# Kernel optimization log

Hardware: AMD Instinct MI355X
Metric: run time of the kernel (lower is better)

## Reference

```python
import jax, jax.numpy as jnp
import numpy as np

B, C, H, W = 8, 64, 56, 56
PLANES = 64
EPS = 1e-5


def conv2d(x, w, b, stride=1, pad=1):
    out = jax.lax.conv_general_dilated(
        x, w, window_strides=(stride, stride), padding=[(pad, pad), (pad, pad)],
        dimension_numbers=('NCHW', 'OIHW', 'NCHW'))
    return out + b[None, :, None, None]


def _bilinear_gather(img, py, px):
    # img: [C,H,W]; py/px: [K2,Ho,Wo] float sample coords; zero outside bounds
    Ci, Hi, Wi = img.shape
    y0 = jnp.floor(py); x0 = jnp.floor(px)
    wy1 = py - y0; wx1 = px - x0
    wy0 = 1.0 - wy1; wx0 = 1.0 - wx1

    def g(yc, xc):
        valid = ((yc >= 0) & (yc < Hi) & (xc >= 0) & (xc < Wi)).astype(img.dtype)
        yi = jnp.clip(yc, 0, Hi - 1).astype(jnp.int32)
        xi = jnp.clip(xc, 0, Wi - 1).astype(jnp.int32)
        return img[:, yi, xi] * valid[None]  # [C,K2,Ho,Wo]

    return (g(y0, x0) * (wy0 * wx0)[None] + g(y0, x0 + 1) * (wy0 * wx1)[None]
            + g(y0 + 1, x0) * (wy1 * wx0)[None] + g(y0 + 1, x0 + 1) * (wy1 * wx1)[None])


def deform_conv2d(x, offset, weight, stride, pad, dil):
    # torchvision DeformConv2d semantics (no mask). offset: [B, 2*K2, Ho, Wo]
    Bx, Cx, Hx, Wx = x.shape
    O, _, kh, kw = weight.shape
    K2 = kh * kw
    Ho, Wo = offset.shape[2], offset.shape[3]
    off = offset.reshape(Bx, K2, 2, Ho, Wo)
    dy, dx = off[:, :, 0], off[:, :, 1]
    ki, kj = jnp.meshgrid(jnp.arange(kh), jnp.arange(kw), indexing='ij')
    base_y = (ki.reshape(-1) * dil - pad).astype(x.dtype)  # [K2]
    base_x = (kj.reshape(-1) * dil - pad).astype(x.dtype)
    hg = (jnp.arange(Ho) * stride).astype(x.dtype)
    wg = (jnp.arange(Wo) * stride).astype(x.dtype)
    py = dy + base_y[None, :, None, None] + hg[None, None, :, None]
    px = dx + base_x[None, :, None, None] + wg[None, None, None, :]
    cols = jax.vmap(_bilinear_gather)(x, py, px)  # [B,C,K2,Ho,Wo]
    return jnp.einsum('bckhw,ock->bohw', cols, weight.reshape(O, Cx, K2))


def bn(x, gamma, beta, mean, var):
    inv = gamma / jnp.sqrt(var + EPS)
    return x * inv[None, :, None, None] + (beta - mean * inv)[None, :, None, None]


def setup_inputs() -> dict:
    key = jax.random.key(0)
    ks = jax.random.split(key, 12)
    s = 0.05
    d = {
        'x':   jax.random.normal(ks[0], (B, C, H, W), jnp.float32),
        'ow1': jax.random.normal(ks[1], (2 * 9, C, 3, 3), jnp.float32) * s,
        'ob1': jnp.zeros((2 * 9,), jnp.float32),
        'ow3': jax.random.normal(ks[2], (2 * 25, C, 3, 3), jnp.float32) * s,
        'ob3': jnp.zeros((2 * 25,), jnp.float32),
        'ow2': jax.random.normal(ks[3], (2 * 9, PLANES, 3, 3), jnp.float32) * s,
        'ob2': jnp.zeros((2 * 9,), jnp.float32),
        'w1':  jax.random.normal(ks[4], (PLANES, C, 3, 3), jnp.float32) * s,
        'w3':  jax.random.normal(ks[5], (PLANES, C, 5, 5), jnp.float32) * s,
        'w2':  jax.random.normal(ks[6], (PLANES, PLANES, 3, 3), jnp.float32) * s,
    }
    for i, tag in zip((7, 8, 9), ('1', '3', '2')):
        d['g' + tag] = jnp.ones((PLANES,), jnp.float32)
        d['b' + tag] = jnp.zeros((PLANES,), jnp.float32)
        d['m' + tag] = jax.random.normal(ks[i], (PLANES,), jnp.float32) * 0.1
        d['v' + tag] = jnp.ones((PLANES,), jnp.float32)
    return d


def reference(x, ow1, ob1, ow3, ob3, ow2, ob2, w1, w3, w2,
              g1, b1, m1, v1, g3, b3, m3, v3, g2, b2, m2, v2):
    offset1 = conv2d(x, ow1, ob1, stride=1, pad=1)
    out = jax.nn.relu(bn(deform_conv2d(x, offset1, w1, 1, 2, 2), g1, b1, m1, v1))
    offset3 = conv2d(x, ow3, ob3, stride=1, pad=1)
    out_1 = jax.nn.relu(bn(deform_conv2d(x, offset3, w3, 1, 4, 2), g3, b3, m3, v3))
    out = out + out_1
    offset2 = conv2d(out, ow2, ob2, stride=1, pad=1)
    out = bn(deform_conv2d(out, offset2, w2, 1, 2, 2), g2, b2, m2, v2)
    out = out + x  # identity shortcut (stride=1, in_planes==planes)
    return jax.nn.relu(out)
```

## Files before the change

### kernel.cpp

```cpp
#include <hip/hip_runtime.h>
#include <math.h>

#define HD 56
#define WD 56
#define CD 64
#define PLANE 3136

typedef _Float16 f16x8 __attribute__((ext_vector_type(8)));
typedef _Float16 f16x4 __attribute__((ext_vector_type(4)));
typedef _Float16 f16x2 __attribute__((ext_vector_type(2)));
typedef float    f32x4 __attribute__((ext_vector_type(4)));

__global__ __launch_bounds__(256) void wtrans_k(
    const float* __restrict__ w1, const float* __restrict__ w3, const float* __restrict__ w2,
    const float* __restrict__ ow1, const float* __restrict__ ow3, const float* __restrict__ ow2,
    _Float16* __restrict__ t1, _Float16* __restrict__ t3, _Float16* __restrict__ t2,
    _Float16* __restrict__ owF, _Float16* __restrict__ owT2)
{
    int y = blockIdx.y;
    if (y == 0 || y == 1 || y == 2) {
        const float* src = (y == 0) ? w1 : (y == 1) ? w3 : w2;
        _Float16* dst    = (y == 0) ? t1 : (y == 1) ? t3 : t2;
        int K2 = (y == 1) ? 25 : 9;
        int total = 64 * 64 * K2;
        for (int idx = blockIdx.x * 256 + threadIdx.x; idx < total; idx += gridDim.x * 256) {
            int k = idx >> 12;
            int o = (idx >> 6) & 63;
            int c = idx & 63;
            dst[idx] = (_Float16)src[(o * 64 + c) * K2 + k];
        }
    } else if (y == 3) {
        int total = 9 * 32 * 64;
        for (int idx = blockIdx.x * 256 + threadIdx.x; idx < total; idx += gridDim.x * 256) {
            int k = idx >> 11;
            int o = (idx >> 6) & 31;
            int c = idx & 63;
            owF[k * 6144 + o * 64 + c] = (o < 18) ? (_Float16)ow1[(o * 64 + c) * 9 + k] : (_Float16)0.f;
        }
    } else if (y == 4) {
        int total = 9 * 64 * 64;
        for (int idx = blockIdx.x * 256 + threadIdx.x; idx < total; idx += gridDim.x * 256) {
            int k = idx >> 12;
            int o = (idx >> 6) & 63;
            int c = idx & 63;
            owF[k * 6144 + (32 + o) * 64 + c] = (o < 50) ? (_Float16)ow3[(o * 64 + c) * 9 + k] : (_Float16)0.f;
        }
    } else {
        int total = 9 * 32 * 64;
        for (int idx = blockIdx.x * 256 + threadIdx.x; idx < total; idx += gridDim.x * 256) {
            int k = idx >> 11;
            int o = (idx >> 6) & 31;
            int c = idx & 63;
            owT2[k * 2048 + o * 64 + c] = (o < 18) ? (_Float16)ow2[(o * 64 + c) * 9 + k] : (_Float16)0.f;
        }
    }
}

__global__ __launch_bounds__(256) void xt_k(const float* __restrict__ src, _Float16* __restrict__ dst)
{
    int b  = blockIdx.y;
    int px = blockIdx.x * 64 + (threadIdx.x & 63);
    int cg = threadIdx.x >> 6;
    const float* s = src + (size_t)b * CD * PLANE + px;
    f16x8 lo, hi;
#pragma unroll
    for (int i = 0; i < 8; ++i) lo[i] = (_Float16)s[(cg * 16 + i) * PLANE];
#pragma unroll
    for (int i = 0; i < 8; ++i) hi[i] = (_Float16)s[(cg * 16 + 8 + i) * PLANE];
    _Float16* d = dst + ((size_t)b * PLANE + px) * 64 + cg * 16;
    *(f16x8*)d = lo;
    *(f16x8*)(d + 8) = hi;
}

template<int NTILES, int OP>
__device__ inline void af_load(const _Float16* __restrict__ ow, int k, int off, f16x8* s) {
    const _Float16* wk = ow + k * (OP * 64);
#pragma unroll
    for (int t = 0; t < NTILES; ++t) s[t] = *(const f16x8*)(wk + (t * 16) * 64 + off);
}

template<int FUSED>
__global__ __launch_bounds__(256) void offc_k(
    const _Float16* __restrict__ src,
    const _Float16* __restrict__ ow,
    const float* __restrict__ biasA, const float* __restrict__ biasB,
    uint4* __restrict__ tbl)
{
    constexpr int NTILES = FUSED ? 6 : 2;
    constexpr int OP     = FUSED ? 96 : 32;
    constexpr int NTT    = FUSED ? 34 : 9;
    __shared__ float red[4][NTILES * 4 * 64];

    int tid = threadIdx.x;
    int bid = blockIdx.x;
    int b    = bid & 7;
    int tile = bid >> 3;
    int l = tid & 63;
    int n = l & 15;
    int g = l >> 4;
    int w = tid >> 6;
    int tg = w >> 1;
    int pix = tile * 16 + n;
    int ho = pix / WD, wo = pix - ho * WD;
    int ckoff = (w & 1) * 32 + g * 8;
    int afo = n * 64 + ckoff;
    const _Float16* sp = src + ((size_t)b * PLANE + pix) * 64 + ckoff;

    f32x4 acc[NTILES];
#pragma unroll
    for (int t = 0; t < NTILES; ++t) acc[t] = (f32x4){0.f, 0.f, 0.f, 0.f};

#define NB(K, D) { int ky_=(K)/3-1, kx_=(K)%3-1; int yn_=ho+ky_, xn_=wo+kx_;       \
    f16x8 z_ = {(_Float16)0,(_Float16)0,(_Float16)0,(_Float16)0,                   \
                (_Float16)0,(_Float16)0,(_Float16)0,(_Float16)0};                  \
    D = z_;                                                                        \
    if ((unsigned)yn_ < (unsigned)HD && (unsigned)xn_ < (unsigned)WD)              \
        D = *(const f16x8*)(sp + (ky_ * WD + kx_) * 64); }

#define MFMAS(S, NBV) { _Pragma("unroll")                                          \
    for (int t = 0; t < NTILES; ++t)                                               \
        acc[t] = __builtin_amdgcn_mfma_f32_16x16x32_f16((S)[t], NBV, acc[t], 0, 0, 0); }

    f16x8 sA[NTILES], sB[NTILES];
    if (tg == 0) {
        f16x8 nb0, nb1, nb2, nb3, nb4;
        NB(0, nb0) NB(1, nb1) NB(2, nb2) NB(3, nb3) NB(4, nb4)
        af_load<NTILES, OP>(ow, 0, afo, sA);
        af_load<NTILES, OP>(ow, 1, afo, sB); MFMAS(sA, nb0)
        af_load<NTILES, OP>(ow, 2, afo, sA); MFMAS(sB, nb1)
        af_load<NTILES, OP>(ow, 3, afo, sB); MFMAS(sA, nb2)
        af_load<NTILES, OP>(ow, 4, afo, sA); MFMAS(sB, nb3)
        MFMAS(sA, nb4)
    } else {
        f16x8 nb0, nb1, nb2, nb3;
        NB(5, nb0) NB(6, nb1) NB(7, nb2) NB(8, nb3)
        af_load<NTILES, OP>(ow, 5, afo, sA);
        af_load<NTILES, OP>(ow, 6, afo, sB); MFMAS(sA, nb0)
        af_load<NTILES, OP>(ow, 7, afo, sA); MFMAS(sB, nb1)
        af_load<NTILES, OP>(ow, 8, afo, sB); MFMAS(sA, nb2)
        MFMAS(sB, nb3)
    }
#undef NB
#undef MFMAS

#pragma unroll
    for (int t = 0; t < NTILES; ++t)
#pragma unroll
        for (int rr = 0; rr < 4; ++rr)
            red[w][(t * 4 + rr) * 64 + l] = acc[t][rr];
    __syncthreads();

#pragma unroll
    for (int tt = 0; tt < (NTILES + 3) / 4; ++tt) {
        int t = w + tt * 4;
        if (t < NTILES) {
            float v[4];
#pragma unroll
            for (int rr = 0; rr < 4; ++rr) {
                int ia = (t * 4 + rr) * 64 + l;
                v[rr] = red[0][ia] + red[1][ia] + red[2][ia] + red[3][ia];
            }
            int obase = t * 16 + g * 4;
            bool isB = FUSED && (t >= 2);
            int oc0 = isB ? (obase - 32) : obase;
            const float* bp = isB ? biasB : biasA;
#pragma unroll
            for (int pp = 0; pp < 2; ++pp) {
                int oce = oc0 + pp * 2;
                int kl  = oce >> 1;
                int kmax = isB ? 25 : 9;
                if (kl < kmax) {
                    float dy = v[pp * 2]     + bp[oce];
                    float dx = v[pp * 2 + 1] + bp[oce + 1];
                    int by, bx;
                    if (isB) { int q = kl / 5; by = q * 2 - 4; bx = (kl - q * 5) * 2 - 4; }
                    else     { int q = kl / 3; by = q * 2 - 2; bx = (kl - q * 3) * 2 - 2; }
                    float py = dy + (float)(by + ho);
                    float px = dx + (float)(bx + wo);
                    float fy = floorf(py), fx = floorf(px);
                    float wy1 = py - fy, wx1 = px - fx;
                    float wy0 = 1.f - wy1, wx0 = 1.f - wx1;
                    int y0 = (int)fy, x0 = (int)fx;
                    int y1 = y0 + 1, x1 = x0 + 1;
                    float vy0 = (y0 >= 0 && y0 < HD) ? 1.f : 0.f;
                    float vy1 = (y1 >= 0 && y1 < HD) ? 1.f : 0.f;
                    float vx0 = (x0 >= 0 && x0 < WD) ? 1.f : 0.f;
                    float vx1 = (x1 >= 0 && x1 < WD) ? 1.f : 0.f;
                    int cy0 = min(max(y0, 0), HD - 1), cy1 = min(max(y1, 0), HD - 1);
                    int cx0 = min(max(x0, 0), WD - 1), cx1 = min(max(x1, 0), WD - 1);
                    unsigned i00 = (unsigned)(cy0 * WD + cx0), i01 = (unsigned)(cy0 * WD + cx1);
                    unsigned i10 = (unsigned)(cy1 * WD + cx0), i11 = (unsigned)(cy1 * WD + cx1);
                    f16x2 wl = {(_Float16)(wy0 * wx0 * vy0 * vx0), (_Float16)(wy0 * wx1 * vy0 * vx1)};
                    f16x2 wh = {(_Float16)(wy1 * wx0 * vy1 * vx0), (_Float16)(wy1 * wx1 * vy1 * vx1)};
                    uint4 e;
                    e.x = i00 | (i01 << 16);
                    e.y = i10 | (i11 << 16);
                    e.z = __builtin_bit_cast(unsigned int, wl);
                    e.w = __builtin_bit_cast(unsigned int, wh);
                    int gtap = isB ? (9 + kl) : kl;
                    tbl[((size_t)(b * NTT + gtap)) * PLANE + pix] = e;
                }
            }
        }
    }
}

template<int MERGED>
__global__ __launch_bounds__(512) void dconv_k(
    const _Float16* __restrict__ xt,
    const uint4* __restrict__ tbl,
    const _Float16* __restrict__ wTA, const _Float16* __restrict__ wTB,
    const float* __restrict__ gA, const float* __restrict__ bA,
    const float* __restrict__ mA, const float* __restrict__ vA,
    const float* __restrict__ gB, const float* __restrict__ bB,
    const float* __restrict__ mB, const float* __restrict__ vB,
    const float* __restrict__ addsrc, float* __restrict__ out,
    _Float16* __restrict__ outh)
{
    constexpr int NT = MERGED ? 34 : 9;
    constexpr int RS = MERGED ? 32 : 16;
    __shared__ float red[2][3][RS * 64];

    int tid = threadIdx.x;
    int bid = blockIdx.x;
    int b    = bid & 7;
    int tp2  = bid >> 3;
    int l   = tid & 63;
    int n   = l & 15;
    int g   = l >> 4;
    int w   = tid >> 6;
    int pr  = w & 1;
    int kh  = (w >> 1) & 1;
    int tg  = w >> 2;
    int tile = tp2 * 2 + pr;
    int pix = tile * 16 + n;
    int ckoff = kh * 32 + g * 8;

    int base, cnt;
    if (MERGED) { base = tg * 17; cnt = 17; }
    else        { base = tg ? 5 : 0; cnt = tg ? 4 : 5; }

    const _Float16* xp = xt + (size_t)b * PLANE * 64 + ckoff;
    const uint4*    tp = tbl + (size_t)b * NT * PLANE + pix;
    int afoff = n * 64 + ckoff;

    f32x4 accA[4], accB[4];
#pragma unroll
    for (int ot = 0; ot < 4; ++ot) {
        accA[ot] = (f32x4){0.f, 0.f, 0.f, 0.f};
        accB[ot] = (f32x4){0.f, 0.f, 0.f, 0.f};
    }

    f16x8 v00, v01, v10, v11, af0, af1, af2, af3;
    _Float16 w0, w1, w2, w3;
    uint4 e_cur;

    {
        uint4 e0 = tp[base * PLANE];
        int t1 = (cnt > 1) ? base + 1 : base;
        e_cur = tp[t1 * PLANE];
        unsigned i00 = e0.x & 0xffffu, i01 = e0.x >> 16;
        unsigned i10 = e0.y & 0xffffu, i11 = e0.y >> 16;
        v00 = *(const f16x8*)(xp + i00 * 64);
        v01 = *(const f16x8*)(xp + i01 * 64);
        v10 = *(const f16x8*)(xp + i10 * 64);
        v11 = *(const f16x8*)(xp + i11 * 64);
        const _Float16* wk = (!MERGED || base < 9) ? (wTA + base * 4096) : (wTB + (base - 9) * 4096);
        af0 = *(const f16x8*)(wk + afoff);
        af1 = *(const f16x8*)(wk + afoff + 1024);
        af2 = *(const f16x8*)(wk + afoff + 2048);
        af3 = *(const f16x8*)(wk + afoff + 3072);
        f16x2 wl = __builtin_bit_cast(f16x2, e0.z);
        f16x2 wh = __builtin_bit_cast(f16x2, e0.w);
        w0 = wl.x; w1 = wl.y; w2 = wh.x; w3 = wh.y;
    }

#pragma unroll 2
    for (int j = 0; j < cnt; ++j) {
        int tap = base + j;
        bool hn = (j + 1 < cnt);
        f16x8 nv00, nv01, nv10, nv11, naf0, naf1, naf2, naf3;
        uint4 e_nxt;
        if (hn) {
            int t2 = (j + 2 < cnt) ? (tap + 2) : (base + cnt - 1);
            e_nxt = tp[t2 * PLANE];
            unsigned i00 = e_cur.x & 0xffffu, i01 = e_cur.x >> 16;
            unsigned i10 = e_cur.y & 0xffffu, i11 = e_cur.y >> 16;
            nv00 = *(const f16x8*)(xp + i00 * 64);
            nv01 = *(const f16x8*)(xp + i01 * 64);
            nv10 = *(const f16x8*)(xp + i10 * 64);
            nv11 = *(const f16x8*)(xp + i11 * 64);
            const _Float16* wk = (!MERGED || tap + 1 < 9) ? (wTA + (tap + 1) * 4096)
                                                          : (wTB + (tap - 8) * 4096);
            naf0 = *(const f16x8*)(wk + afoff);
            naf1 = *(const f16x8*)(wk + afoff + 1024);
            naf2 = *(const f16x8*)(wk + afoff + 2048);
            naf3 = *(const f16x8*)(wk + afoff + 3072);
        }
        f16x8 bf = v00 * w0 + v01 * w1 + v10 * w2 + v11 * w3;
        if (!MERGED || tap < 9) {
            accA[0] = __builtin_amdgcn_mfma_f32_16x16x32_f16(af0, bf, accA[0], 0, 0, 0);
            accA[1] = __builtin_amdgcn_mfma_f32_16x16x32_f16(af1, bf, accA[1], 0, 0, 0);
            accA[2] = __builtin_amdgcn_mfma_f32_16x16x32_f16(af2, bf, accA[2], 0, 0, 0);
            accA[3] = __builtin_amdgcn_mfma_f32_16x16x32_f16(af3, bf, accA[3], 0, 0, 0);
        } else {
            accB[0] = __builtin_amdgcn_mfma_f32_16x16x32_f16(af0, bf, accB[0], 0, 0, 0);
            accB[1] = __builtin_amdgcn_mfma_f32_16x16x32_f16(af1, bf, accB[1], 0, 0, 0);
            accB[2] = __builtin_amdgcn_mfma_f32_16x16x32_f16(af2, bf, accB[2], 0, 0, 0);
            accB[3] = __builtin_amdgcn_mfma_f32_16x16x32_f16(af3, bf, accB[3], 0, 0, 0);
        }
        if (hn) {
            v00 = nv00; v01 = nv01; v10 = nv10; v11 = nv11;
            af0 = naf0; af1 = naf1; af2 = naf2; af3 = naf3;
            f16x2 wl = __builtin_bit_cast(f16x2, e_cur.z);
            f16x2 wh = __builtin_bit_cast(f16x2, e_cur.w);
            w0 = wl.x; w1 = wl.y; w2 = wh.x; w3 = wh.y;
            e_cur = e_nxt;
        }
    }

    int pidx = (tg << 1) | kh;
    if (pidx > 0) {
#pragma unroll
        for (int ot = 0; ot < 4; ++ot)
#pragma unroll
            for (int rr = 0; rr < 4; ++rr) {
                red[pr][pidx - 1][(ot * 4 + rr) * 64 + l] = accA[ot][rr];
                if (MERGED) red[pr][pidx - 1][(16 + ot * 4 + rr) * 64 + l] = accB[ot][rr];
            }
    }
    __syncthreads();
    if (pidx == 0) {
#pragma unroll
        for (int ot = 0; ot < 4; ++ot) {
            float r[4];
#pragma unroll
            for (int rr = 0; rr < 4; ++rr) {
                int ia = (ot * 4 + rr) * 64 + l;
                int o = ot * 16 + g * 4 + rr;
                if (MERGED) {
                    int ib = (16 + ot * 4 + rr) * 64 + l;
                    float sumA = accA[ot][rr] + red[pr][0][ia] + red[pr][1][ia] + red[pr][2][ia];
                    float sumB = accB[ot][rr] + red[pr][0][ib] + red[pr][1][ib] + red[pr][2][ib];
                    float ivA = gA[o] * (1.f / sqrtf(vA[o] + 1e-5f));
                    float shA = bA[o] - mA[o] * ivA;
                    float ivB = gB[o] * (1.f / sqrtf(vB[o] + 1e-5f));
                    float shB = bB[o] - mB[o] * ivB;
                    r[rr] = fmaxf(sumA * ivA + shA, 0.f) + fmaxf(sumB * ivB + shB, 0.f);
                } else {
                    float s = accA[ot][rr] + red[pr][0][ia] + red[pr][1][ia] + red[pr][2][ia];
                    float iv = gA[o] * (1.f / sqrtf(vA[o] + 1e-5f));
                    float sh = bA[o] - mA[o] * iv;
                    size_t oidx = (size_t)(b * 64 + o) * PLANE + pix;
                    out[oidx] = fmaxf(s * iv + sh + addsrc[oidx], 0.f);
                }
            }
            if (MERGED) {
                f16x4 hv = {(_Float16)r[0], (_Float16)r[1], (_Float16)r[2], (_Float16)r[3]};
                *(f16x4*)(outh + ((size_t)b * PLANE + pix) * 64 + ot * 16 + g * 4) = hv;
            }
        }
    }
}

extern "C" void kernel_launch(void* const* d_in, const int* in_sizes, int n_in,
                              void* d_out, int out_size, void* d_ws, size_t ws_size,
                              hipStream_t stream) {
    const float* x   = (const float*)d_in[0];
    const float* ow1 = (const float*)d_in[1];
    const float* ob1 = (const float*)d_in[2];
    const float* ow3 = (const float*)d_in[3];
    const float* ob3 = (const float*)d_in[4];
    const float* ow2 = (const float*)d_in[5];
    const float* ob2 = (const float*)d_in[6];
    const float* w1  = (const float*)d_in[7];
    const float* w3  = (const float*)d_in[8];
    const float* w2  = (const float*)d_in[9];
    const float* g1  = (const float*)d_in[10];
    const float* b1  = (const float*)d_in[11];
    const float* m1  = (const float*)d_in[12];
    const float* v1  = (const float*)d_in[13];
    const float* g3  = (const float*)d_in[14];
    const float* b3  = (const float*)d_in[15];
    const float* m3  = (const float*)d_in[16];
    const float* v3  = (const float*)d_in[17];
    const float* g2  = (const float*)d_in[18];
    const float* b2  = (const float*)d_in[19];
    const float* m2  = (const float*)d_in[20];
    const float* v2  = (const float*)d_in[21];

    float* out = (float*)d_out;
    float* ws  = (float*)d_ws;

    _Float16* xth  = (_Float16*)ws;
    _Float16* mth  = (_Float16*)(ws + 802816);
    uint4*    tbl  = (uint4*)(ws + 1605632);
    _Float16* wT1h = (_Float16*)(ws + 5017600);
    _Float16* wT3h = wT1h + 36864;
    _Float16* wT2h = wT3h + 102400;
    _Float16* owFh = wT2h + 36864;
    _Float16* owT2h= owFh + 55296;

    wtrans_k<<<dim3(16, 6), dim3(256), 0, stream>>>(
        w1, w3, w2, ow1, ow3, ow2, wT1h, wT3h, wT2h, owFh, owT2h);
    xt_k<<<dim3(49, 8), dim3(256), 0, stream>>>(x, xth);

    offc_k<1><<<dim3(1568), dim3(256), 0, stream>>>(xth, owFh, ob1, ob3, tbl);

    dconv_k<1><<<dim3(784), dim3(512), 0, stream>>>(
        xth, tbl, wT1h, wT3h, g1, b1, m1, v1, g3, b3, m3, v3, nullptr, nullptr, mth);

    offc_k<0><<<dim3(1568), dim3(256), 0, stream>>>(mth, owT2h, ob2, ob2, tbl);

    dconv_k<0><<<dim3(784), dim3(512), 0, stream>>>(
        mth, tbl, wT2h, wT2h, g2, b2, m2, v2, g2, b2, m2, v2, x, out, nullptr);
}
```

Baseline: 219.3 us.

## Process two pixel tiles per wave to reuse weight fragments across MFMAs

Each wave in the deformable conv kernel now handles two 16-pixel tiles and shares one set of loaded weight A-fragments between them, halving weight loads per MFMA. Block sizes drop to 384 and 256 threads. The merged kernel splits taps unevenly (9, 12 and 13) so that each wave group accumulates only branch A or only branch B, which removes the dual accumulator set. This costs more registers per thread for the doubled gathered values and accumulators, and there are fewer waves per block to hide gather latency.

```diff
diff --git a/kernel.cpp b/kernel.cpp
--- a/kernel.cpp
+++ b/kernel.cpp
@@ -206,7 +206,7 @@
 }
 
 template<int MERGED>
-__global__ __launch_bounds__(512) void dconv_k(
+__global__ __launch_bounds__(MERGED ? 384 : 256) void dconv_k(
     const _Float16* __restrict__ xt,
     const uint4* __restrict__ tbl,
     const _Float16* __restrict__ wTA, const _Float16* __restrict__ wTB,
@@ -218,146 +218,154 @@
     _Float16* __restrict__ outh)
 {
     constexpr int NT = MERGED ? 34 : 9;
-    constexpr int RS = MERGED ? 32 : 16;
-    __shared__ float red[2][3][RS * 64];
+    constexpr int NP = MERGED ? 5 : 3;
+    __shared__ float red[NP][2][16 * 64];
 
     int tid = threadIdx.x;
     int bid = blockIdx.x;
     int b    = bid & 7;
     int tp2  = bid >> 3;
-    int l   = tid & 63;
-    int n   = l & 15;
-    int g   = l >> 4;
-    int w   = tid >> 6;
-    int pr  = w & 1;
-    int kh  = (w >> 1) & 1;
-    int tg  = w >> 2;
-    int tile = tp2 * 2 + pr;
-    int pix = tile * 16 + n;
+    int l = tid & 63, n = l & 15, g = l >> 4;
+    int w = tid >> 6;
+    int kh = w & 1;
+    int tg = w >> 1;
+    int pix0 = tp2 * 32 + n;
     int ckoff = kh * 32 + g * 8;
 
     int base, cnt;
-    if (MERGED) { base = tg * 17; cnt = 17; }
-    else        { base = tg ? 5 : 0; cnt = tg ? 4 : 5; }
+    bool isA;
+    if (MERGED) {
+        base = (tg == 0) ? 0 : (tg == 1) ? 9 : 21;
+        cnt  = (tg == 0) ? 9 : (tg == 1) ? 12 : 13;
+        isA  = (tg == 0);
+    } else {
+        base = tg ? 5 : 0; cnt = tg ? 4 : 5; isA = true;
+    }
+    const _Float16* wTb = isA ? wTA : wTB;
+    int kofs = isA ? 0 : 9;
 
     const _Float16* xp = xt + (size_t)b * PLANE * 64 + ckoff;
-    const uint4*    tp = tbl + (size_t)b * NT * PLANE + pix;
+    const uint4* tpp = tbl + (size_t)b * NT * PLANE + pix0;
     int afoff = n * 64 + ckoff;
 
-    f32x4 accA[4], accB[4];
-#pragma unroll
-    for (int ot = 0; ot < 4; ++ot) {
-        accA[ot] = (f32x4){0.f, 0.f, 0.f, 0.f};
-        accB[ot] = (f32x4){0.f, 0.f, 0.f, 0.f};
-    }
-
-    f16x8 v00, v01, v10, v11, af0, af1, af2, af3;
-    _Float16 w0, w1, w2, w3;
-    uint4 e_cur;
+    f32x4 acc[2][4];
+#pragma unroll
+    for (int t = 0; t < 2; ++t)
+#pragma unroll
+        for (int q = 0; q < 4; ++q) acc[t][q] = (f32x4){0.f, 0.f, 0.f, 0.f};
+
+    f16x8 v[2][4], af4[4];
+    uint4 ecur[2];
+    unsigned wz[2], ww[2];
 
     {
-        uint4 e0 = tp[base * PLANE];
+        uint4 e00 = tpp[base * PLANE];
+        uint4 e01 = tpp[base * PLANE + 16];
         int t1 = (cnt > 1) ? base + 1 : base;
-        e_cur = tp[t1 * PLANE];
-        unsigned i00 = e0.x & 0xffffu, i01 = e0.x >> 16;
-        unsigned i10 = e0.y & 0xffffu, i11 = e0.y >> 16;
-        v00 = *(const f16x8*)(xp + i00 * 64);
-        v01 = *(const f16x8*)(xp + i01 * 64);
-        v10 = *(const f16x8*)(xp + i10 * 64);
-        v11 = *(const f16x8*)(xp + i11 * 64);
-        const _Float16* wk = (!MERGED || base < 9) ? (wTA + base * 4096) : (wTB + (base - 9) * 4096);
-        af0 = *(const f16x8*)(wk + afoff);
-        af1 = *(const f16x8*)(wk + afoff + 1024);
-        af2 = *(const f16x8*)(wk + afoff + 2048);
-        af3 = *(const f16x8*)(wk + afoff + 3072);
-        f16x2 wl = __builtin_bit_cast(f16x2, e0.z);
-        f16x2 wh = __builtin_bit_cast(f16x2, e0.w);
-        w0 = wl.x; w1 = wl.y; w2 = wh.x; w3 = wh.y;
+        ecur[0] = tpp[t1 * PLANE];
+        ecur[1] = tpp[t1 * PLANE + 16];
+        uint4 ee[2] = {e00, e01};
+#pragma unroll
+        for (int t = 0; t < 2; ++t) {
+            unsigned i00 = ee[t].x & 0xffffu, i01 = ee[t].x >> 16;
+            unsigned i10 = ee[t].y & 0xffffu, i11 = ee[t].y >> 16;
+            v[t][0] = *(const f16x8*)(xp + i00 * 64);
+            v[t][1] = *(const f16x8*)(xp + i01 * 64);
+            v[t][2] = *(const f16x8*)(xp + i10 * 64);
+            v[t][3] = *(const f16x8*)(xp + i11 * 64);
+            wz[t] = ee[t].z; ww[t] = ee[t].w;
+        }
+        const _Float16* wk = wTb + (base - kofs) * 4096;
+#pragma unroll
+        for (int q = 0; q < 4; ++q) af4[q] = *(const f16x8*)(wk + afoff + q * 1024);
     }
 
 #pragma unroll 2
     for (int j = 0; j < cnt; ++j) {
         int tap = base + j;
         bool hn = (j + 1 < cnt);
-        f16x8 nv00, nv01, nv10, nv11, naf0, naf1, naf2, naf3;
-        uint4 e_nxt;
+        f16x8 nv[2][4], naf[4];
+        uint4 enxt[2];
         if (hn) {
             int t2 = (j + 2 < cnt) ? (tap + 2) : (base + cnt - 1);
-            e_nxt = tp[t2 * PLANE];
-            unsigned i00 = e_cur.x & 0xffffu, i01 = e_cur.x >> 16;
-            unsigned i10 = e_cur.y & 0xffffu, i11 = e_cur.y >> 16;
-            nv00 = *(const f16x8*)(xp + i00 * 64);
-            nv01 = *(const f16x8*)(xp + i01 * 64);
-            nv10 = *(const f16x8*)(xp + i10 * 64);
-            nv11 = *(const f16x8*)(xp + i11 * 64);
-            const _Float16* wk = (!MERGED || tap + 1 < 9) ? (wTA + (tap + 1) * 4096)
-                                                          : (wTB + (tap - 8) * 4096);
-            naf0 = *(const f16x8*)(wk + afoff);
-            naf1 = *(const f16x8*)(wk + afoff + 1024);
-            naf2 = *(const f16x8*)(wk + afoff + 2048);
-            naf3 = *(const f16x8*)(wk + afoff + 3072);
-        }
-        f16x8 bf = v00 * w0 + v01 * w1 + v10 * w2 + v11 * w3;
-        if (!MERGED || tap < 9) {
-            accA[0] = __builtin_amdgcn_mfma_f32_16x16x32_f16(af0, bf, accA[0], 0, 0, 0);
-            accA[1] = __builtin_amdgcn_mfma_f32_16x16x32_f16(af1, bf, accA[1], 0, 0, 0);
-            accA[2] = __builtin_amdgcn_mfma_f32_16x16x32_f16(af2, bf, accA[2], 0, 0, 0);
-            accA[3] = __builtin_amdgcn_mfma_f32_16x16x32_f16(af3, bf, accA[3], 0, 0, 0);
-        } else {
-            accB[0] = __builtin_amdgcn_mfma_f32_16x16x32_f16(af0, bf, accB[0], 0, 0, 0);
-            accB[1] = __builtin_amdgcn_mfma_f32_16x16x32_f16(af1, bf, accB[1], 0, 0, 0);
-            accB[2] = __builtin_amdgcn_mfma_f32_16x16x32_f16(af2, bf, accB[2], 0, 0, 0);
-            accB[3] = __builtin_amdgcn_mfma_f32_16x16x32_f16(af3, bf, accB[3], 0, 0, 0);
+            enxt[0] = tpp[t2 * PLANE];
+            enxt[1] = tpp[t2 * PLANE + 16];
+#pragma unroll
+            for (int t = 0; t < 2; ++t) {
+                unsigned i00 = ecur[t].x & 0xffffu, i01 = ecur[t].x >> 16;
+                unsigned i10 = ecur[t].y & 0xffffu, i11 = ecur[t].y >> 16;
+                nv[t][0] = *(const f16x8*)(xp + i00 * 64);
+                nv[t][1] = *(const f16x8*)(xp + i01 * 64);
+                nv[t][2] = *(const f16x8*)(xp + i10 * 64);
+                nv[t][3] = *(const f16x8*)(xp + i11 * 64);
+            }
+            const _Float16* wk = wTb + (tap + 1 - kofs) * 4096;
+#pragma unroll
+            for (int q = 0; q < 4; ++q) naf[q] = *(const f16x8*)(wk + afoff + q * 1024);
+        }
+#pragma unroll
+        for (int t = 0; t < 2; ++t) {
+            f16x2 wl = __builtin_bit_cast(f16x2, wz[t]);
+            f16x2 wh = __builtin_bit_cast(f16x2, ww[t]);
+            f16x8 bf = v[t][0] * wl.x + v[t][1] * wl.y + v[t][2] * wh.x + v[t][3] * wh.y;
+#pragma unroll
+            for (int q = 0; q < 4; ++q)
+                acc[t][q] = __builtin_amdgcn_mfma_f32_16x16x32_f16(af4[q], bf, acc[t][q], 0, 0, 0);
         }
         if (hn) {
-            v00 = nv00; v01 = nv01; v10 = nv10; v11 = nv11;
-            af0 = naf0; af1 = naf1; af2 = naf2; af3 = naf3;
-            f16x2 wl = __builtin_bit_cast(f16x2, e_cur.z);
-            f16x2 wh = __builtin_bit_cast(f16x2, e_cur.w);
-            w0 = wl.x; w1 = wl.y; w2 = wh.x; w3 = wh.y;
-            e_cur = e_nxt;
-        }
-    }
-
-    int pidx = (tg << 1) | kh;
-    if (pidx > 0) {
-#pragma unroll
-        for (int ot = 0; ot < 4; ++ot)
-#pragma unroll
-            for (int rr = 0; rr < 4; ++rr) {
-                red[pr][pidx - 1][(ot * 4 + rr) * 64 + l] = accA[ot][rr];
-                if (MERGED) red[pr][pidx - 1][(16 + ot * 4 + rr) * 64 + l] = accB[ot][rr];
+#pragma unroll
+            for (int t = 0; t < 2; ++t) {
+#pragma unroll
+                for (int c = 0; c < 4; ++c) v[t][c] = nv[t][c];
+                wz[t] = ecur[t].z; ww[t] = ecur[t].w;
+                ecur[t] = enxt[t];
             }
+#pragma unroll
+            for (int q = 0; q < 4; ++q) af4[q] = naf[q];
+        }
+    }
+
+    if (w > 0) {
+#pragma unroll
+        for (int t = 0; t < 2; ++t)
+#pragma unroll
+            for (int ot = 0; ot < 4; ++ot)
+#pragma unroll
+                for (int rr = 0; rr < 4; ++rr)
+                    red[w - 1][t][(ot * 4 + rr) * 64 + l] = acc[t][ot][rr];
     }
     __syncthreads();
-    if (pidx == 0) {
-#pragma unroll
-        for (int ot = 0; ot < 4; ++ot) {
-            float r[4];
-#pragma unroll
-            for (int rr = 0; rr < 4; ++rr) {
-                int ia = (ot * 4 + rr) * 64 + l;
-                int o = ot * 16 + g * 4 + rr;
+    if (w == 0) {
+#pragma unroll
+        for (int t = 0; t < 2; ++t) {
+            int pix = pix0 + t * 16;
+#pragma unroll
+            for (int ot = 0; ot < 4; ++ot) {
+                float r[4];
+#pragma unroll
+                for (int rr = 0; rr < 4; ++rr) {
+                    int ia = (ot * 4 + rr) * 64 + l;
+                    int o = ot * 16 + g * 4 + rr;
+                    if (MERGED) {
+                        float sumA = acc[t][ot][rr] + red[0][t][ia];
+                        float sumB = red[1][t][ia] + red[2][t][ia] + red[3][t][ia] + red[4][t][ia];
+                        float ivA = gA[o] * (1.f / sqrtf(vA[o] + 1e-5f));
+                        float shA = bA[o] - mA[o] * ivA;
+                        float ivB = gB[o] * (1.f / sqrtf(vB[o] + 1e-5f));
+                        float shB = bB[o] - mB[o] * ivB;
+                        r[rr] = fmaxf(sumA * ivA + shA, 0.f) + fmaxf(sumB * ivB + shB, 0.f);
+                    } else {
+                        float s = acc[t][ot][rr] + red[0][t][ia] + red[1][t][ia] + red[2][t][ia];
+                        float iv = gA[o] * (1.f / sqrtf(vA[o] + 1e-5f));
+                        float sh = bA[o] - mA[o] * iv;
+                        size_t oidx = (size_t)(b * 64 + o) * PLANE + pix;
+                        out[oidx] = fmaxf(s * iv + sh + addsrc[oidx], 0.f);
+                    }
+                }
                 if (MERGED) {
-                    int ib = (16 + ot * 4 + rr) * 64 + l;
-                    float sumA = accA[ot][rr] + red[pr][0][ia] + red[pr][1][ia] + red[pr][2][ia];
-                    float sumB = accB[ot][rr] + red[pr][0][ib] + red[pr][1][ib] + red[pr][2][ib];
-                    float ivA = gA[o] * (1.f / sqrtf(vA[o] + 1e-5f));
-                    float shA = bA[o] - mA[o] * ivA;
-                    float ivB = gB[o] * (1.f / sqrtf(vB[o] + 1e-5f));
-                    float shB = bB[o] - mB[o] * ivB;
-                    r[rr] = fmaxf(sumA * ivA + shA, 0.f) + fmaxf(sumB * ivB + shB, 0.f);
-                } else {
-                    float s = accA[ot][rr] + red[pr][0][ia] + red[pr][1][ia] + red[pr][2][ia];
-                    float iv = gA[o] * (1.f / sqrtf(vA[o] + 1e-5f));
-                    float sh = bA[o] - mA[o] * iv;
-                    size_t oidx = (size_t)(b * 64 + o) * PLANE + pix;
-                    out[oidx] = fmaxf(s * iv + sh + addsrc[oidx], 0.f);
+                    f16x4 hv = {(_Float16)r[0], (_Float16)r[1], (_Float16)r[2], (_Float16)r[3]};
+                    *(f16x4*)(outh + ((size_t)b * PLANE + pix) * 64 + ot * 16 + g * 4) = hv;
                 }
-            }
-            if (MERGED) {
-                f16x4 hv = {(_Float16)r[0], (_Float16)r[1], (_Float16)r[2], (_Float16)r[3]};
-                *(f16x4*)(outh + ((size_t)b * PLANE + pix) * 64 + ot * 16 + g * 4) = hv;
             }
         }
     }
@@ -407,11 +415,11 @@
 
     offc_k<1><<<dim3(1568), dim3(256), 0, stream>>>(xth, owFh, ob1, ob3, tbl);
 
-    dconv_k<1><<<dim3(784), dim3(512), 0, stream>>>(
+    dconv_k<1><<<dim3(784), dim3(384), 0, stream>>>(
         xth, tbl, wT1h, wT3h, g1, b1, m1, v1, g3, b3, m3, v3, nullptr, nullptr, mth);
 
     offc_k<0><<<dim3(1568), dim3(256), 0, stream>>>(mth, owT2h, ob2, ob2, tbl);
 
-    dconv_k<0><<<dim3(784), dim3(512), 0, stream>>>(
+    dconv_k<0><<<dim3(784), dim3(256), 0, stream>>>(
         mth, tbl, wT2h, wT2h, g2, b2, m2, v2, g2, b2, m2, v2, x, out, nullptr);
 }
```

After: 231.0 us. 5.3% more time.
